# Kernel optimization log

Hardware: AMD Instinct MI355X
Metric: run time of the kernel (lower is better)

## Reference

```python
import jax, jax.numpy as jnp
import numpy as np

K = 3          # kernel size (both dims)
PAD = 1        # padding used both for offset_mask conv and deform_conv2d
KK = K * K


def setup_inputs() -> dict:
    key = jax.random.key(0)
    k0, k1, k2, k3, k4 = jax.random.split(key, 5)
    B, C, H, W, O = 8, 64, 64, 64, 64
    input_feat = jax.random.normal(k0, (B, C, H, W), jnp.float32)
    degrad_inter = jax.random.normal(k1, (B, C, H, W), jnp.float32)
    stdv = 1.0 / np.sqrt(C * K * K)
    weight = jax.random.uniform(k2, (O, C, K, K), jnp.float32, -stdv, stdv)
    # small-magnitude offset/mask conv params -> realistic small learned offsets
    om_weight = jax.random.normal(k3, (3 * KK, 2 * C, K, K), jnp.float32) * 0.01
    om_bias = jax.random.normal(k4, (3 * KK,), jnp.float32) * 0.01
    return {"input_feat": input_feat, "degrad_inter": degrad_inter,
            "weight": weight, "om_weight": om_weight, "om_bias": om_bias}


def _conv2d(x, w, b):
    out = jax.lax.conv_general_dilated(
        x, w, window_strides=(1, 1), padding=((PAD, PAD), (PAD, PAD)),
        dimension_numbers=("NCHW", "OIHW", "NCHW"))
    return out + b[None, :, None, None]


def _deform_conv2d(x, offset, mask, weight):
    # x: (B,C,H,W); offset: (B,2*KK,H,W) with channel 2k=dy_k, 2k+1=dx_k;
    # mask: (B,KK,H,W); weight: (O,C,K,K). stride=1, padding=PAD, dilation=1.
    B, C, H, W = x.shape
    O = weight.shape[0]
    off = offset.reshape(B, KK, 2, H, W)
    dy, dx = off[:, :, 0], off[:, :, 1]                       # (B,KK,H,W)

    ky, kx = jnp.meshgrid(jnp.arange(K), jnp.arange(K), indexing="ij")
    ky = ky.reshape(KK).astype(x.dtype)
    kx = kx.reshape(KK).astype(x.dtype)
    hh = jnp.arange(H, dtype=x.dtype)
    ww = jnp.arange(W, dtype=x.dtype)
    # absolute fractional sample locations: (B,KK,H,W)
    y = hh[None, None, :, None] - PAD + ky[None, :, None, None] + dy
    xq = ww[None, None, None, :] - PAD + kx[None, :, None, None] + dx

    y0 = jnp.floor(y).astype(jnp.int32)
    x0 = jnp.floor(xq).astype(jnp.int32)
    y1, x1 = y0 + 1, x0 + 1
    wy = y - y0.astype(x.dtype)
    wx = xq - x0.astype(x.dtype)

    x_flat = x.reshape(B, C, H * W)

    def gather(yi, xi):
        valid = (yi >= 0) & (yi < H) & (xi >= 0) & (xi < W)
        idx = jnp.clip(yi, 0, H - 1) * W + jnp.clip(xi, 0, W - 1)  # (B,KK,H,W)
        vals = jax.vmap(lambda im, ix: im[:, ix])(x_flat, idx)     # (B,C,KK,H,W)
        return vals * valid[:, None].astype(x.dtype)

    wy_ = wy[:, None]  # (B,1,KK,H,W)
    wx_ = wx[:, None]
    sampled = (gather(y0, x0) * (1 - wy_) * (1 - wx_)
               + gather(y0, x1) * (1 - wy_) * wx_
               + gather(y1, x0) * wy_ * (1 - wx_)
               + gather(y1, x1) * wy_ * wx_)                       # (B,C,KK,H,W)
    sampled = sampled * mask[:, None]
    return jnp.einsum("bckhw,ock->bohw", sampled, weight.reshape(O, C, KK))


def reference(input_feat, degrad_inter, weight, om_weight, om_bias):
    concat = jnp.concatenate([input_feat, degrad_inter], axis=1)
    om = _conv2d(concat, om_weight, om_bias)                       # (B,3*KK,H,W)
    off1, off2, mask = jnp.split(om, 3, axis=1)
    offset = jnp.concatenate([off1, off2], axis=1)                 # (B,2*KK,H,W)
    mask = jax.nn.sigmoid(mask)                                    # (B,KK,H,W)
    return _deform_conv2d(input_feat, offset, mask, weight)
```

## Files before the change

### kernel.cpp

```cpp
#include <hip/hip_runtime.h>
#include <math.h>

#define WO_PK_OFF 36864
#define CATT_OFF  73728

typedef short  short8  __attribute__((ext_vector_type(8)));
typedef float  float4v __attribute__((ext_vector_type(4)));

static __device__ __forceinline__ short f2bf(float f) {
    unsigned int u = __builtin_bit_cast(unsigned int, f);
    u += 0x7FFFu + ((u >> 16) & 1u);
    return (short)(u >> 16);
}
static __device__ __forceinline__ float bf2f(unsigned short u) {
    return __builtin_bit_cast(float, (unsigned int)u << 16);
}

__global__ __launch_bounds__(256) void prep_transpose(
    const float* __restrict__ feat, const float* __restrict__ deg,
    const float* __restrict__ weight, const float* __restrict__ om_weight,
    unsigned short* __restrict__ catT,
    short* __restrict__ wd_pk, short* __restrict__ wo_pk)
{
    __shared__ unsigned short T[64 * 136];
    const int tid = threadIdx.x;
    if (blockIdx.x < 512) {
        const int b = blockIdx.x >> 6, h = blockIdx.x & 63;
        const int lane = tid & 63, wv = tid >> 6;
#pragma unroll
        for (int cc = 0; cc < 32; cc++) {
            int c = wv * 32 + cc;
            const float* src = (c < 64)
                ? (feat + (size_t)(b * 64 + c) * 4096)
                : (deg  + (size_t)(b * 64 + (c - 64)) * 4096);
            T[lane * 136 + c] = (unsigned short)f2bf(src[h * 64 + lane]);
        }
        __syncthreads();
        const int px = tid >> 2, seg = tid & 3;
        unsigned short* dst =
            catT + (size_t)(b * 4096 + h * 64 + px) * 128 + seg * 32;
#pragma unroll
        for (int j = 0; j < 4; j++)
            *(uint4*)(dst + j * 8) = *(const uint4*)&T[px * 136 + seg * 32 + j * 8];
    } else {
        int idx = (blockIdx.x - 512) * 256 + tid;
        if (idx < 36864) {
            int j = idx & 7, o = (idx >> 3) & 63;
            int lq = (idx >> 9) & 3, ks = idx >> 11;
            int t = ks >> 1, c = (ks & 1) * 32 + lq * 8 + j;
            wd_pk[idx] = f2bf(weight[(o * 64 + c) * 9 + t]);
        } else {
            int e = idx - 36864;
            int j = e & 7, oc = (e >> 3) & 31;
            int lq = (e >> 8) & 3, ks2 = e >> 10;
            int quarter = ks2 / 9, t = ks2 - quarter * 9;
            int cg = quarter * 32 + lq * 8 + j;
            wo_pk[e] = (oc < 27) ? f2bf(om_weight[(oc * 128 + cg) * 9 + t])
                                 : (short)0;
        }
    }
}

__global__ __launch_bounds__(256, 2) void fused_kernel(
    const unsigned short* __restrict__ catT, const short* __restrict__ wd_pk,
    const short* __restrict__ wo_pk, const float* __restrict__ om_bias,
    float* __restrict__ out)
{
    __shared__ float T[4 * 576];
    const int tid = threadIdx.x;
    const int lane = tid & 63, wv = tid >> 6;
    const int l16 = lane & 15, lq = lane >> 4;
    const int gw = blockIdx.x * 4 + wv;
    const int b = gw >> 8, tile = gw & 255;
    const int h = tile >> 2, w0 = (tile & 3) << 4;
    const int pxx = w0 + l16;
    const unsigned short* cb = catT + (size_t)b * 4096 * 128;
    const short8 zf = {0, 0, 0, 0, 0, 0, 0, 0};

    auto loadB1 = [&](int s) -> short8 {
        int quarter = s / 9, t = s - quarter * 9;
        int ky = t / 3, kx = t - ky * 3;
        int yy = h - 1 + ky, xx = pxx - 1 + kx;
        bool ok = (yy >= 0) & (yy <= 63) & (xx >= 0) & (xx <= 63);
        int yc = min(max(yy, 0), 63), xc = min(max(xx, 0), 63);
        short8 v = *(const short8*)(cb + (yc * 64 + xc) * 128
                                       + quarter * 32 + lq * 8);
        return ok ? v : zf;
    };
    float4v oacc0 = {0.f, 0.f, 0.f, 0.f};
    float4v oacc1 = {0.f, 0.f, 0.f, 0.f};
    short8 b1 = loadB1(0);
#pragma unroll
    for (int s = 0; s < 36; s++) {
        short8 bn = zf;
        if (s + 1 < 36) bn = loadB1(s + 1);
        const short8* Ap = (const short8*)(wo_pk + (size_t)(s * 4 + lq) * 256);
        oacc0 = __builtin_amdgcn_mfma_f32_16x16x32_bf16(Ap[l16], b1, oacc0, 0, 0, 0);
        oacc1 = __builtin_amdgcn_mfma_f32_16x16x32_bf16(Ap[16 + l16], b1, oacc1, 0, 0, 0);
        b1 = bn;
    }

    float* Tw = T + wv * 576;
#pragma unroll
    for (int r = 0; r < 4; r++) {
        Tw[l16 * 36 + lq * 4 + r]      = oacc0[r];
        Tw[l16 * 36 + 16 + lq * 4 + r] = oacc1[r];
    }
    __syncthreads();
    float omv[28];
#pragma unroll
    for (int jj = 0; jj < 7; jj++)
        *(float4v*)&omv[jj * 4] = *(const float4v*)&Tw[l16 * 36 + jj * 4];
#pragma unroll
    for (int j = 0; j < 27; j++) omv[j] += om_bias[j];

    float Wb[9][4];
    int   Ob[9][4];
#pragma unroll
    for (int t = 0; t < 9; t++) {
        const int ky = t / 3, kx = t - ky * 3;
        float dy = omv[2 * t], dx = omv[2 * t + 1];
        float mm = 1.f / (1.f + __expf(-omv[18 + t]));
        float yf = (float)(h - 1 + ky) + dy;
        float xf = (float)(pxx - 1 + kx) + dx;
        float fy = floorf(yf), fx = floorf(xf);
        int y0 = (int)fy, x0 = (int)fx;
        float wy = yf - fy, wx = xf - fx;
        bool vy0 = (y0 >= 0) & (y0 < 64);
        bool vy1 = (y0 >= -1) & (y0 < 63);
        bool vx0 = (x0 >= 0) & (x0 < 64);
        bool vx1 = (x0 >= -1) & (x0 < 63);
        float a0 = (1.f - wy) * mm, a1 = wy * mm;
        Wb[t][0] = a0 * (1.f - wx) * (float)(vy0 & vx0);
        Wb[t][1] = a0 * wx         * (float)(vy0 & vx1);
        Wb[t][2] = a1 * (1.f - wx) * (float)(vy1 & vx0);
        Wb[t][3] = a1 * wx         * (float)(vy1 & vx1);
        int iy0 = min(max(y0, 0), 63),     ix0 = min(max(x0, 0), 63);
        int iy1 = min(max(y0 + 1, 0), 63), ix1 = min(max(x0 + 1, 0), 63);
        Ob[t][0] = (iy0 * 64 + ix0) * 128;  Ob[t][1] = (iy0 * 64 + ix1) * 128;
        Ob[t][2] = (iy1 * 64 + ix0) * 128;  Ob[t][3] = (iy1 * 64 + ix1) * 128;
    }

    float4v acc[4];
#pragma unroll
    for (int mt = 0; mt < 4; mt++) acc[mt] = (float4v){0.f, 0.f, 0.f, 0.f};

    auto loadC = [&](int s, short8* c) {
        int t = s >> 1, qh = s & 1;
        int cho = qh * 32 + lq * 8;
#pragma unroll
        for (int r = 0; r < 4; r++)
            c[r] = *(const short8*)(cb + Ob[t][r] + cho);
    };
    short8 cur[4], nxt[4];
    loadC(0, cur);
#pragma unroll
    for (int s = 0; s < 18; s++) {
        if (s + 1 < 18) loadC(s + 1, nxt);
        const int t = s >> 1;
        short8 bfr;
#pragma unroll
        for (int j = 0; j < 8; j++) {
            float v = Wb[t][0] * bf2f((unsigned short)cur[0][j])
                    + Wb[t][1] * bf2f((unsigned short)cur[1][j])
                    + Wb[t][2] * bf2f((unsigned short)cur[2][j])
                    + Wb[t][3] * bf2f((unsigned short)cur[3][j]);
            bfr[j] = f2bf(v);
        }
        const short8* Dp = (const short8*)(wd_pk + (size_t)(s * 4 + lq) * 512);
        acc[0] = __builtin_amdgcn_mfma_f32_16x16x32_bf16(Dp[l16],      bfr, acc[0], 0, 0, 0);
        acc[1] = __builtin_amdgcn_mfma_f32_16x16x32_bf16(Dp[16 + l16], bfr, acc[1], 0, 0, 0);
        acc[2] = __builtin_amdgcn_mfma_f32_16x16x32_bf16(Dp[32 + l16], bfr, acc[2], 0, 0, 0);
        acc[3] = __builtin_amdgcn_mfma_f32_16x16x32_bf16(Dp[48 + l16], bfr, acc[3], 0, 0, 0);
#pragma unroll
        for (int r = 0; r < 4; r++) cur[r] = nxt[r];
    }

    float* ob = out + (size_t)(b * 64) * 4096 + h * 64 + w0 + l16;
#pragma unroll
    for (int mt = 0; mt < 4; mt++)
#pragma unroll
        for (int r = 0; r < 4; r++)
            ob[(mt * 16 + lq * 4 + r) * 4096] = acc[mt][r];
}

extern "C" void kernel_launch(void* const* d_in, const int* in_sizes, int n_in,
                              void* d_out, int out_size, void* d_ws, size_t ws_size,
                              hipStream_t stream)
{
    const float* feat      = (const float*)d_in[0];
    const float* deg       = (const float*)d_in[1];
    const float* weight    = (const float*)d_in[2];
    const float* om_weight = (const float*)d_in[3];
    const float* om_bias   = (const float*)d_in[4];
    float* out = (float*)d_out;
    short* wss = (short*)d_ws;
    unsigned short* catT = (unsigned short*)(wss + CATT_OFF);

    hipLaunchKernelGGL(prep_transpose, dim3(800), dim3(256), 0, stream,
                       feat, deg, weight, om_weight, catT,
                       wss, wss + WO_PK_OFF);
    hipLaunchKernelGGL(fused_kernel,   dim3(512), dim3(256), 0, stream,
                       catT, wss, wss + WO_PK_OFF, om_bias, out);
}
```

Before: 119.8 us.

## Merge prep and fused kernels into one cooperative kernel with grid sync

```diff
diff --git a/kernel.cpp b/kernel.cpp
--- a/kernel.cpp
+++ b/kernel.cpp
@@ -1,5 +1,8 @@
 #include <hip/hip_runtime.h>
+#include <hip/hip_cooperative_groups.h>
 #include <math.h>
+
+namespace cg = cooperative_groups;
 
 #define WO_PK_OFF 36864
 #define CATT_OFF  73728
@@ -16,17 +19,20 @@
     return __builtin_bit_cast(float, (unsigned int)u << 16);
 }
 
-__global__ __launch_bounds__(256) void prep_transpose(
+__global__ __launch_bounds__(256, 2) void mono_kernel(
     const float* __restrict__ feat, const float* __restrict__ deg,
     const float* __restrict__ weight, const float* __restrict__ om_weight,
+    const float* __restrict__ om_bias,
     unsigned short* __restrict__ catT,
-    short* __restrict__ wd_pk, short* __restrict__ wo_pk)
+    short* __restrict__ wd_pk, short* __restrict__ wo_pk,
+    float* __restrict__ out)
 {
     __shared__ unsigned short T[64 * 136];
     const int tid = threadIdx.x;
-    if (blockIdx.x < 512) {
+    const int lane = tid & 63, wv = tid >> 6;
+
+    {
         const int b = blockIdx.x >> 6, h = blockIdx.x & 63;
-        const int lane = tid & 63, wv = tid >> 6;
 #pragma unroll
         for (int cc = 0; cc < 32; cc++) {
             int c = wv * 32 + cc;
@@ -35,6 +41,23 @@
                 : (deg  + (size_t)(b * 64 + (c - 64)) * 4096);
             T[lane * 136 + c] = (unsigned short)f2bf(src[h * 64 + lane]);
         }
+        if (blockIdx.x < 288) {
+            int idx = blockIdx.x * 256 + tid;
+            if (idx < 36864) {
+                int j = idx & 7, o = (idx >> 3) & 63;
+                int lq2 = (idx >> 9) & 3, ks = idx >> 11;
+                int t = ks >> 1, c = (ks & 1) * 32 + lq2 * 8 + j;
+                wd_pk[idx] = f2bf(weight[(o * 64 + c) * 9 + t]);
+            } else {
+                int e = idx - 36864;
+                int j = e & 7, oc = (e >> 3) & 31;
+                int lq2 = (e >> 8) & 3, ks2 = e >> 10;
+                int quarter = ks2 / 9, t = ks2 - quarter * 9;
+                int cg2 = quarter * 32 + lq2 * 8 + j;
+                wo_pk[e] = (oc < 27) ? f2bf(om_weight[(oc * 128 + cg2) * 9 + t])
+                                     : (short)0;
+            }
+        }
         __syncthreads();
         const int px = tid >> 2, seg = tid & 3;
         unsigned short* dst =
@@ -42,33 +65,10 @@
 #pragma unroll
         for (int j = 0; j < 4; j++)
             *(uint4*)(dst + j * 8) = *(const uint4*)&T[px * 136 + seg * 32 + j * 8];
-    } else {
-        int idx = (blockIdx.x - 512) * 256 + tid;
-        if (idx < 36864) {
-            int j = idx & 7, o = (idx >> 3) & 63;
-            int lq = (idx >> 9) & 3, ks = idx >> 11;
-            int t = ks >> 1, c = (ks & 1) * 32 + lq * 8 + j;
-            wd_pk[idx] = f2bf(weight[(o * 64 + c) * 9 + t]);
-        } else {
-            int e = idx - 36864;
-            int j = e & 7, oc = (e >> 3) & 31;
-            int lq = (e >> 8) & 3, ks2 = e >> 10;
-            int quarter = ks2 / 9, t = ks2 - quarter * 9;
-            int cg = quarter * 32 + lq * 8 + j;
-            wo_pk[e] = (oc < 27) ? f2bf(om_weight[(oc * 128 + cg) * 9 + t])
-                                 : (short)0;
-        }
-    }
-}
-
-__global__ __launch_bounds__(256, 2) void fused_kernel(
-    const unsigned short* __restrict__ catT, const short* __restrict__ wd_pk,
-    const short* __restrict__ wo_pk, const float* __restrict__ om_bias,
-    float* __restrict__ out)
-{
-    __shared__ float T[4 * 576];
-    const int tid = threadIdx.x;
-    const int lane = tid & 63, wv = tid >> 6;
+    }
+    __threadfence();
+    cg::this_grid().sync();
+
     const int l16 = lane & 15, lq = lane >> 4;
     const int gw = blockIdx.x * 4 + wv;
     const int b = gw >> 8, tile = gw & 255;
@@ -89,18 +89,19 @@
     };
     float4v oacc0 = {0.f, 0.f, 0.f, 0.f};
     float4v oacc1 = {0.f, 0.f, 0.f, 0.f};
-    short8 b1 = loadB1(0);
+    short8 pb[3];
+    pb[0] = loadB1(0); pb[1] = loadB1(1); pb[2] = loadB1(2);
 #pragma unroll
     for (int s = 0; s < 36; s++) {
-        short8 bn = zf;
-        if (s + 1 < 36) bn = loadB1(s + 1);
+        short8 bcur = pb[s % 3];
+        if (s + 3 < 36) pb[s % 3] = loadB1(s + 3);
         const short8* Ap = (const short8*)(wo_pk + (size_t)(s * 4 + lq) * 256);
-        oacc0 = __builtin_amdgcn_mfma_f32_16x16x32_bf16(Ap[l16], b1, oacc0, 0, 0, 0);
-        oacc1 = __builtin_amdgcn_mfma_f32_16x16x32_bf16(Ap[16 + l16], b1, oacc1, 0, 0, 0);
-        b1 = bn;
-    }
-
-    float* Tw = T + wv * 576;
+        oacc0 = __builtin_amdgcn_mfma_f32_16x16x32_bf16(Ap[l16],      bcur, oacc0, 0, 0, 0);
+        oacc1 = __builtin_amdgcn_mfma_f32_16x16x32_bf16(Ap[16 + l16], bcur, oacc1, 0, 0, 0);
+    }
+
+    float* Tw = (float*)T + wv * 576;
+    __syncthreads();
 #pragma unroll
     for (int r = 0; r < 4; r++) {
         Tw[l16 * 36 + lq * 4 + r]      = oacc0[r];
@@ -152,11 +153,12 @@
         for (int r = 0; r < 4; r++)
             c[r] = *(const short8*)(cb + Ob[t][r] + cho);
     };
-    short8 cur[4], nxt[4];
-    loadC(0, cur);
+    short8 cb0[4], cb1[4];
+    loadC(0, cb0);
+    loadC(1, cb1);
 #pragma unroll
     for (int s = 0; s < 18; s++) {
-        if (s + 1 < 18) loadC(s + 1, nxt);
+        short8* cur = (s & 1) ? cb1 : cb0;
         const int t = s >> 1;
         short8 bfr;
 #pragma unroll
@@ -167,13 +169,12 @@
                     + Wb[t][3] * bf2f((unsigned short)cur[3][j]);
             bfr[j] = f2bf(v);
         }
+        if (s + 2 < 18) loadC(s + 2, cur);
         const short8* Dp = (const short8*)(wd_pk + (size_t)(s * 4 + lq) * 512);
         acc[0] = __builtin_amdgcn_mfma_f32_16x16x32_bf16(Dp[l16],      bfr, acc[0], 0, 0, 0);
         acc[1] = __builtin_amdgcn_mfma_f32_16x16x32_bf16(Dp[16 + l16], bfr, acc[1], 0, 0, 0);
         acc[2] = __builtin_amdgcn_mfma_f32_16x16x32_bf16(Dp[32 + l16], bfr, acc[2], 0, 0, 0);
         acc[3] = __builtin_amdgcn_mfma_f32_16x16x32_bf16(Dp[48 + l16], bfr, acc[3], 0, 0, 0);
-#pragma unroll
-        for (int r = 0; r < 4; r++) cur[r] = nxt[r];
     }
 
     float* ob = out + (size_t)(b * 64) * 4096 + h * 64 + w0 + l16;
@@ -195,11 +196,15 @@
     const float* om_bias   = (const float*)d_in[4];
     float* out = (float*)d_out;
     short* wss = (short*)d_ws;
+    short* wd_pk = wss;
+    short* wo_pk = wss + WO_PK_OFF;
     unsigned short* catT = (unsigned short*)(wss + CATT_OFF);
 
-    hipLaunchKernelGGL(prep_transpose, dim3(800), dim3(256), 0, stream,
-                       feat, deg, weight, om_weight, catT,
-                       wss, wss + WO_PK_OFF);
-    hipLaunchKernelGGL(fused_kernel,   dim3(512), dim3(256), 0, stream,
-                       catT, wss, wss + WO_PK_OFF, om_bias, out);
-}
+    void* args[] = {
+        (void*)&feat, (void*)&deg, (void*)&weight, (void*)&om_weight,
+        (void*)&om_bias, (void*)&catT, (void*)&wd_pk, (void*)&wo_pk,
+        (void*)&out
+    };
+    hipLaunchCooperativeKernel((const void*)mono_kernel,
+                               dim3(512), dim3(256), args, 0, stream);
+}
```

Result: slower. 255.2 us (+113.0%).
